# Kernel optimization log

Hardware: AMD Instinct MI355X
Metric: run time of the kernel (lower is better)

Reference implementation:

```python
import jax, jax.numpy as jnp
import numpy as np

H = 12      # num attention heads
W = 128     # one-sided window size (band = 2W+1), also the chunk size
G = 32      # number of global tokens (positions 0..G-1)
NEG = -1e9


def setup_inputs() -> dict:
    key = jax.random.key(0)
    ks = jax.random.split(key, 9)
    B, S, D = 1, 4096, 768
    std = 0.02
    f32 = jnp.float32
    return {
        "hidden_states": jax.random.normal(ks[0], (B, S, D), f32),
        "Wq": jax.random.normal(ks[1], (D, D), f32) * std,
        "bq": jnp.zeros((D,), f32),
        "Wk": jax.random.normal(ks[2], (D, D), f32) * std,
        "bk": jnp.zeros((D,), f32),
        "Wv": jax.random.normal(ks[3], (D, D), f32) * std,
        "bv": jnp.zeros((D,), f32),
        "Wo": jax.random.normal(ks[4], (D, D), f32) * std,
        "bo": jnp.zeros((D,), f32),
    }


def _longformer_attn(hidden, Wq, bq, Wk, bk, Wv, bv, Wo, bo):
    B, S, D = hidden.shape
    dh = D // H
    scale = jnp.asarray(dh, hidden.dtype) ** -0.5

    def proj(Wm, bm):
        return (hidden @ Wm + bm).reshape(B, S, H, dh).transpose(0, 2, 1, 3)  # [B,H,S,dh]

    q = proj(Wq, bq) * scale
    k = proj(Wk, bk)
    v = proj(Wv, bv)

    nc = S // W  # number of query chunks
    q_ch = q.reshape(B, H, nc, W, dh)

    # pad keys/values by one chunk on each side; chunk c sees keys [c*W - W, c*W + 2W)
    kp = jnp.pad(k, ((0, 0), (0, 0), (W, W), (0, 0)))
    vp = jnp.pad(v, ((0, 0), (0, 0), (W, W), (0, 0)))
    idx = (jnp.arange(nc) * W)[:, None] + jnp.arange(3 * W)[None, :]  # [nc, 3W] into padded seq
    k_ch = kp[:, :, idx]  # [B,H,nc,3W,dh]
    v_ch = vp[:, :, idx]

    # banded scores via chunked matmul: [B,H,nc,W,3W]
    band = jnp.einsum('bhcqd,bhckd->bhcqk', q_ch, k_ch)

    # exact band mask |i-j| <= W: with local query qi and local key kj (global j = c*W + kj - W)
    qi = jnp.arange(W)[:, None]           # [W,1]
    kj = jnp.arange(3 * W)[None, :]       # [1,3W]
    in_band = (kj >= qi) & (kj <= qi + 2 * W)                     # [W,3W]
    j = (jnp.arange(nc) * W)[:, None, None] + kj[None] - W        # [nc,1,3W] global key index
    valid = in_band[None] & (j >= G) & (j < S)                    # [nc,W,3W]; j<G handled via global path
    band = jnp.where(valid[None, None], band, NEG)
    band = band.reshape(B, H, S, 3 * W)

    # every query also attends to the G global keys
    gsc = jnp.einsum('bhsd,bhgd->bhsg', q, k[:, :, :G])           # [B,H,S,G]
    scores = jnp.concatenate([gsc, band], axis=-1)                # [B,H,S,G+3W]
    probs = jax.nn.softmax(scores, axis=-1)

    out = jnp.einsum('bhsg,bhgd->bhsd', probs[..., :G], v[:, :, :G])
    pb = probs[..., G:].reshape(B, H, nc, W, 3 * W)
    out = out + jnp.einsum('bhcqk,bhckd->bhcqd', pb, v_ch).reshape(B, H, S, dh)

    # global queries attend to everything (full attention on G rows)
    gq_probs = jax.nn.softmax(jnp.einsum('bhgd,bhsd->bhgs', q[:, :, :G], k), axis=-1)
    out_g = jnp.einsum('bhgs,bhsd->bhgd', gq_probs, v)
    out = out.at[:, :, :G].set(out_g)

    out = out.transpose(0, 2, 1, 3).reshape(B, S, D)
    return out @ Wo + bo


def reference(hidden_states, Wq, bq, Wk, bk, Wv, bv, Wo, bo):
    return _longformer_attn(hidden_states, Wq, bq, Wk, bk, Wv, bv, Wo, bo)
```

## Files before the change

### kernel.cpp

```cpp
#include <hip/hip_runtime.h>
#include <stdint.h>

#define S_LEN 4096
#define DMOD  768
#define NH    12
#define DH    64
#define GG    32
#define NEGBIG (-1e9f)

typedef _Float16 f16;
typedef f16 f16x8 __attribute__((ext_vector_type(8)));
typedef f16 f16x4 __attribute__((ext_vector_type(4)));
typedef float f32x4 __attribute__((ext_vector_type(4)));
typedef uint32_t u32;

#define OFF_H16   ((size_t)0)
#define OFF_WT    ((size_t)6291456)
#define OFF_Q     ((size_t)11010048)
#define OFF_K     ((size_t)17301504)
#define OFF_VT    ((size_t)29884416)
#define OFF_ATT   ((size_t)36175872)
#define OFF_GQO   ((size_t)42467328)
#define OFF_GQL   ((size_t)44040192)

__device__ __forceinline__ void gld_lds16(const void* g, void* l) {
  typedef __attribute__((address_space(3))) u32 lds_u32;
  typedef __attribute__((address_space(1))) u32 glb_u32;
  __builtin_amdgcn_global_load_lds((glb_u32*)(uintptr_t)g,
                                   (lds_u32*)(u32)(uintptr_t)l, 16, 0, 0);
}

__global__ __launch_bounds__(256) void prep_kernel(
    const float* __restrict__ hs,
    const float* __restrict__ Wq, const float* __restrict__ Wk,
    const float* __restrict__ Wv, const float* __restrict__ Wo,
    f16* __restrict__ h16, f16* __restrict__ wt)
{
  const int b = blockIdx.x;
  const int t = threadIdx.x;
  if (b < 576) {
    __shared__ float tile[64][65];
    const int w = b / 144, r2 = b % 144;
    const int n0 = (r2 % 12) * 64, k0 = (r2 / 12) * 64;
    const float* W = (w==0) ? Wq : (w==1) ? Wk : (w==2) ? Wv : Wo;
    f16* WT = wt + (size_t)w * DMOD * DMOD;
    #pragma unroll
    for (int rnd = 0; rnd < 4; ++rnd) {
      const int lin = rnd * 1024 + t * 4;
      const int r = lin >> 6, c = lin & 63;
      const float4 vv = *(const float4*)(W + (size_t)(k0 + r) * DMOD + n0 + c);
      tile[r][c+0] = vv.x; tile[r][c+1] = vv.y; tile[r][c+2] = vv.z; tile[r][c+3] = vv.w;
    }
    __syncthreads();
    #pragma unroll
    for (int rnd = 0; rnd < 2; ++rnd) {
      const int lin = rnd * 256 + t;
      const int n = lin >> 3, kc = (lin & 7) * 8;
      f16x8 o;
      #pragma unroll
      for (int j = 0; j < 8; ++j) o[j] = (f16)tile[kc + j][n];
      *(f16x8*)(WT + (size_t)(n0 + n) * DMOD + k0 + kc) = o;
    }
  } else {
    const size_t idx = (size_t)(b - 576) * 2048 + (size_t)t * 8;
    const float4 a = *(const float4*)(hs + idx);
    const float4 c = *(const float4*)(hs + idx + 4);
    f16x8 o;
    o[0]=(f16)a.x; o[1]=(f16)a.y; o[2]=(f16)a.z; o[3]=(f16)a.w;
    o[4]=(f16)c.x; o[5]=(f16)c.y; o[6]=(f16)c.z; o[7]=(f16)c.w;
    *(f16x8*)(h16 + idx) = o;
  }
}

__global__ __launch_bounds__(256) void gemm_qkv(
    const f16* __restrict__ A, const f16* __restrict__ wt,
    const float* __restrict__ bq, const float* __restrict__ bk, const float* __restrict__ bv,
    f16* __restrict__ q16, f16* __restrict__ k16, f16* __restrict__ vt16)
{
  __shared__ __align__(16) f16 At[3][4096];
  __shared__ __align__(16) f16 Bt[3][4096];
  const int z = blockIdx.z;
  const f16* Wt = wt + (size_t)z * DMOD * DMOD;
  const float* bias = (z==0) ? bq : (z==1) ? bk : bv;
  const float scale = (z==0) ? 0.125f : 1.0f;

  const int tid = threadIdx.x;
  const int lane = tid & 63, wid = tid >> 6;
  const int quad = lane >> 4, l15 = lane & 15;
  const int n0 = blockIdx.x * 128, m0 = blockIdx.y * 128;
  const int wm = (wid >> 1) * 64, wn = (wid & 1) * 64;

  f32x4 acc[4][4];
  #pragma unroll
  for (int i=0;i<4;++i)
    #pragma unroll
    for (int j=0;j<4;++j) acc[i][j] = (f32x4){0.f,0.f,0.f,0.f};

  const int lin0 = tid, lin1 = tid + 256;
  const int ar0 = ((lin0>>6)<<4) + (lin0&15), ac0 = ((lin0>>4)&3)*8;
  const int ar1 = ((lin1>>6)<<4) + (lin1&15), ac1 = ((lin1>>4)&3)*8;
  const f16* Ab = A  + (size_t)m0 * DMOD;
  const f16* Bb = Wt + (size_t)n0 * DMOD;

  #pragma unroll
  for (int p = 0; p < 2; ++p) {
    const int k0 = p * 32;
    gld_lds16(Ab + (size_t)ar0*DMOD + k0 + ac0, &At[p][lin0*8]);
    gld_lds16(Ab + (size_t)ar1*DMOD + k0 + ac1, &At[p][lin1*8]);
    gld_lds16(Bb + (size_t)ar0*DMOD + k0 + ac0, &Bt[p][lin0*8]);
    gld_lds16(Bb + (size_t)ar1*DMOD + k0 + ac1, &Bt[p][lin1*8]);
  }

  #pragma unroll 3
  for (int k = 0; k < 24; ++k) {
    const int cb = k % 3, ib = (k + 2) % 3;
    if (k < 23) {
      asm volatile("s_waitcnt vmcnt(4) lgkmcnt(0)" ::: "memory");
    } else {
      asm volatile("s_waitcnt vmcnt(0) lgkmcnt(0)" ::: "memory");
    }
    __builtin_amdgcn_s_barrier();
    if (k < 22) {
      const int k0 = (k + 2) * 32;
      gld_lds16(Ab + (size_t)ar0*DMOD + k0 + ac0, &At[ib][lin0*8]);
      gld_lds16(Ab + (size_t)ar1*DMOD + k0 + ac1, &At[ib][lin1*8]);
      gld_lds16(Bb + (size_t)ar0*DMOD + k0 + ac0, &Bt[ib][lin0*8]);
      gld_lds16(Bb + (size_t)ar1*DMOD + k0 + ac1, &Bt[ib][lin1*8]);
    }
    f16x8 af[4], bf[4];
    #pragma unroll
    for (int i=0;i<4;++i) {
      af[i] = *(const f16x8*)(&At[cb][((wm>>4)+i)*512 + lane*8]);
      bf[i] = *(const f16x8*)(&Bt[cb][((wn>>4)+i)*512 + lane*8]);
    }
    #pragma unroll
    for (int i=0;i<4;++i)
      #pragma unroll
      for (int j=0;j<4;++j)
        acc[i][j] = __builtin_amdgcn_mfma_f32_16x16x32_f16(af[i], bf[j], acc[i][j], 0, 0, 0);
  }

  if (z < 2) {
    f16* outp = (z==0) ? q16 : k16;
    #pragma unroll
    for (int j=0;j<4;++j) {
      const int col = n0 + wn + j*16 + l15;
      const float bcol = bias[col];
      const int h = col >> 6, d = col & 63;
      #pragma unroll
      for (int i=0;i<4;++i) {
        const int rbase = m0 + wm + i*16 + quad*4;
        f16* dst = outp + ((size_t)h * S_LEN + rbase) * DH + d;
        #pragma unroll
        for (int r=0;r<4;++r)
          dst[(size_t)r * DH] = (f16)((acc[i][j][r] + bcol) * scale);
      }
    }
  } else {
    #pragma unroll
    for (int j=0;j<4;++j) {
      const int col = n0 + wn + j*16 + l15;
      const float bcol = bias[col];
      const int h = col >> 6, d = col & 63;
      #pragma unroll
      for (int i=0;i<4;++i) {
        const int rbase = m0 + wm + i*16 + quad*4;
        f16x4 o;
        #pragma unroll
        for (int r=0;r<4;++r) o[r] = (f16)(acc[i][j][r] + bcol);
        *(f16x4*)(vt16 + ((size_t)h * DH + d) * S_LEN + rbase) = o;
      }
    }
  }
}

__global__ __launch_bounds__(256) void gemm_out(
    const f16* __restrict__ A, const f16* __restrict__ Wt,
    const float* __restrict__ bo, float* __restrict__ outp)
{
  __shared__ __align__(16) f16 At[3][2048];
  __shared__ __align__(16) f16 Bt[3][2048];
  const int tid = threadIdx.x;
  const int lane = tid & 63, wid = tid >> 6;
  const int quad = lane >> 4, l15 = lane & 15;
  const int n0 = blockIdx.x * 64, m0 = blockIdx.y * 64;
  const int wm = (wid >> 1) * 32, wn = (wid & 1) * 32;

  f32x4 acc[2][2];
  #pragma unroll
  for (int i=0;i<2;++i)
    #pragma unroll
    for (int j=0;j<2;++j) acc[i][j] = (f32x4){0.f,0.f,0.f,0.f};

  const int ar = ((tid>>6)<<4) + (tid&15), ac = ((tid>>4)&3)*8;
  const f16* Ab = A  + (size_t)m0 * DMOD;
  const f16* Bb = Wt + (size_t)n0 * DMOD;

  #pragma unroll
  for (int p = 0; p < 2; ++p) {
    const int k0 = p * 32;
    gld_lds16(Ab + (size_t)ar*DMOD + k0 + ac, &At[p][tid*8]);
    gld_lds16(Bb + (size_t)ar*DMOD + k0 + ac, &Bt[p][tid*8]);
  }

  #pragma unroll 3
  for (int k = 0; k < 24; ++k) {
    const int cb = k % 3, ib = (k + 2) % 3;
    if (k < 23) {
      asm volatile("s_waitcnt vmcnt(2) lgkmcnt(0)" ::: "memory");
    } else {
      asm volatile("s_waitcnt vmcnt(0) lgkmcnt(0)" ::: "memory");
    }
    __builtin_amdgcn_s_barrier();
    if (k < 22) {
      const int k0 = (k + 2) * 32;
      gld_lds16(Ab + (size_t)ar*DMOD + k0 + ac, &At[ib][tid*8]);
      gld_lds16(Bb + (size_t)ar*DMOD + k0 + ac, &Bt[ib][tid*8]);
    }
    f16x8 af[2], bf[2];
    #pragma unroll
    for (int i=0;i<2;++i) {
      af[i] = *(const f16x8*)(&At[cb][((wm>>4)+i)*512 + lane*8]);
      bf[i] = *(const f16x8*)(&Bt[cb][((wn>>4)+i)*512 + lane*8]);
    }
    #pragma unroll
    for (int i=0;i<2;++i)
      #pragma unroll
      for (int j=0;j<2;++j)
        acc[i][j] = __builtin_amdgcn_mfma_f32_16x16x32_f16(af[i], bf[j], acc[i][j], 0, 0, 0);
  }

  #pragma unroll
  for (int j=0;j<2;++j) {
    const int col = n0 + wn + j*16 + l15;
    const float bcol = bo[col];
    #pragma unroll
    for (int i=0;i<2;++i) {
      const int rbase = m0 + wm + i*16 + quad*4;
      #pragma unroll
      for (int r=0;r<4;++r)
        outp[(size_t)(rbase + r) * DMOD + col] = acc[i][j][r] + bcol;
    }
  }
}

__global__ __launch_bounds__(256) void band_attn(
    const f16* __restrict__ q16, const f16* __restrict__ k16,
    const f16* __restrict__ vt16, f16* __restrict__ att16,
    float* __restrict__ o_part, float* __restrict__ l_part)
{
  __shared__ __align__(16) f16 Pbuf[4][1280];
  const int h = blockIdx.y;
  const int tid = threadIdx.x, lane = tid & 63, wid = tid >> 6;
  const int quad = lane >> 4, l15 = lane & 15;
  f16* P = &Pbuf[wid][0];

  const int bx = blockIdx.x;
  const bool is_gq = (bx >= 32);
  int gr0 = 0, sp = 0, tcount;
  if (is_gq) {
    sp = (bx - 32) * 4 + wid;
    tcount = 8;
  } else {
    const int sub = bx * 4 + wid;
    if (sub == 0) return;
    gr0 = sub * 32;
    tcount = 10;
  }

  const f16* qh = q16 + (size_t)h * S_LEN * DH;
  const f16* kh = k16 + (size_t)h * S_LEN * DH;
  const f16* vh = vt16 + (size_t)h * DH * S_LEN;

  f16x8 aq[2][2];
  #pragma unroll
  for (int mt=0;mt<2;++mt)
    #pragma unroll
    for (int ks=0;ks<2;++ks)
      aq[mt][ks] = *(const f16x8*)(qh + (size_t)(gr0 + mt*16 + l15)*DH + ks*32 + quad*8);

  f32x4 accO[2][4];
  float lacc[2][4];
  #pragma unroll
  for (int mt=0;mt<2;++mt) {
    #pragma unroll
    for (int n=0;n<4;++n) accO[mt][n] = (f32x4){0.f,0.f,0.f,0.f};
    #pragma unroll
    for (int r=0;r<4;++r) lacc[mt][r] = 0.f;
  }

  for (int t = 0; t < tcount; ++t) {
    int j0;
    if (is_gq) {
      j0 = sp*256 + t*32;
    } else if (t > 0) {
      j0 = gr0 - 128 + (t-1)*32;
      if (j0 <= 0 || j0 >= S_LEN) continue;
    } else {
      j0 = 0;
    }
    f16x8 bk[2][2];
    #pragma unroll
    for (int nt=0;nt<2;++nt) {
      const int key = j0 + nt*16 + l15;
      #pragma unroll
      for (int ks=0;ks<2;++ks)
        bk[nt][ks] = *(const f16x8*)(kh + (size_t)key*DH + ks*32 + quad*8);
    }
    f32x4 sc[2][2];
    #pragma unroll
    for (int mt=0;mt<2;++mt)
      #pragma unroll
      for (int nt=0;nt<2;++nt) {
        f32x4 s = __builtin_amdgcn_mfma_f32_16x16x32_f16(aq[mt][0], bk[nt][0],
                                                         (f32x4){0.f,0.f,0.f,0.f}, 0,0,0);
        sc[mt][nt] = __builtin_amdgcn_mfma_f32_16x16x32_f16(aq[mt][1], bk[nt][1], s, 0,0,0);
      }
    if (!is_gq && (t == 1 || t == 9)) {
      #pragma unroll
      for (int nt=0;nt<2;++nt)
        #pragma unroll
        for (int mt=0;mt<2;++mt)
          #pragma unroll
          for (int r=0;r<4;++r) {
            const int e = (nt*16 + l15) - (mt*16 + quad*4 + r);
            const bool ok = (t == 1) ? (e >= 0) : (e <= 0);
            if (!ok) sc[mt][nt][r] = NEGBIG;
          }
    }
    #pragma unroll
    for (int mt=0;mt<2;++mt)
      #pragma unroll
      for (int r=0;r<4;++r) {
        sc[mt][0][r] = __expf(sc[mt][0][r]);
        sc[mt][1][r] = __expf(sc[mt][1][r]);
        lacc[mt][r] += sc[mt][0][r] + sc[mt][1][r];
      }
    #pragma unroll
    for (int mt=0;mt<2;++mt)
      #pragma unroll
      for (int nt=0;nt<2;++nt)
        #pragma unroll
        for (int r=0;r<4;++r)
          P[(mt*16 + quad*4 + r)*40 + nt*16 + l15] = (f16)sc[mt][nt][r];
    asm volatile("s_waitcnt lgkmcnt(0)" ::: "memory");
    f16x8 ap[2];
    #pragma unroll
    for (int mt=0;mt<2;++mt)
      ap[mt] = *(const f16x8*)(P + (mt*16 + l15)*40 + quad*8);
    #pragma unroll
    for (int n=0;n<4;++n) {
      const f16x8 bv = *(const f16x8*)(vh + (size_t)(n*16 + l15)*S_LEN + j0 + quad*8);
      #pragma unroll
      for (int mt=0;mt<2;++mt)
        accO[mt][n] = __builtin_amdgcn_mfma_f32_16x16x32_f16(ap[mt], bv, accO[mt][n], 0,0,0);
    }
  }

  #pragma unroll
  for (int mt=0;mt<2;++mt)
    #pragma unroll
    for (int r=0;r<4;++r) {
      float v = lacc[mt][r];
      v += __shfl_xor(v, 1, 64);
      v += __shfl_xor(v, 2, 64);
      v += __shfl_xor(v, 4, 64);
      v += __shfl_xor(v, 8, 64);
      lacc[mt][r] = v;
    }

  if (is_gq) {
    const int base = (h*16 + sp)*32;
    #pragma unroll
    for (int mt=0;mt<2;++mt)
      #pragma unroll
      for (int r=0;r<4;++r) {
        const int row = mt*16 + quad*4 + r;
        if (l15 == 0) l_part[base+row] = lacc[mt][r];
        #pragma unroll
        for (int n=0;n<4;++n)
          o_part[(size_t)(base+row)*DH + n*16 + l15] = accO[mt][n][r];
      }
  } else {
    #pragma unroll
    for (int mt=0;mt<2;++mt)
      #pragma unroll
      for (int r=0;r<4;++r) {
        const float inv = 1.f / lacc[mt][r];
        const int s = gr0 + mt*16 + quad*4 + r;
        #pragma unroll
        for (int n=0;n<4;++n)
          att16[(size_t)s * DMOD + h*DH + n*16 + l15] = (f16)(accO[mt][n][r] * inv);
      }
  }
}

__global__ __launch_bounds__(256) void gq_merge(
    const float* __restrict__ o_part, const float* __restrict__ l_part,
    f16* __restrict__ att16)
{
  const int h = blockIdx.x;
  const int t = threadIdx.x;
  for (int u = t; u < 512; u += 256) {
    const int row = u >> 4, c4 = u & 15;
    float4 s = {0.f,0.f,0.f,0.f};
    float l = 0.f;
    for (int sp=0;sp<16;++sp) {
      const int base = (h*16 + sp)*32 + row;
      const float4 v = *(const float4*)&o_part[(size_t)base*DH + c4*4];
      s.x += v.x; s.y += v.y; s.z += v.z; s.w += v.w;
      l += l_part[base];
    }
    const float inv = 1.f / l;
    f16x4 o;
    o[0] = (f16)(s.x*inv); o[1] = (f16)(s.y*inv);
    o[2] = (f16)(s.z*inv); o[3] = (f16)(s.w*inv);
    *(f16x4*)&att16[(size_t)row * DMOD + h*DH + c4*4] = o;
  }
}

extern "C" void kernel_launch(void* const* d_in, const int* in_sizes, int n_in,
                              void* d_out, int out_size, void* d_ws, size_t ws_size,
                              hipStream_t stream)
{
  const float* hs = (const float*)d_in[0];
  const float* Wq = (const float*)d_in[1];
  const float* bq = (const float*)d_in[2];
  const float* Wk = (const float*)d_in[3];
  const float* bk = (const float*)d_in[4];
  const float* Wv = (const float*)d_in[5];
  const float* bv = (const float*)d_in[6];
  const float* Wo = (const float*)d_in[7];
  const float* bo = (const float*)d_in[8];
  float* out = (float*)d_out;
  char* ws = (char*)d_ws;
  f16* h16  = (f16*)(ws + OFF_H16);
  f16* wt   = (f16*)(ws + OFF_WT);
  f16* q16  = (f16*)(ws + OFF_Q);
  f16* k16  = (f16*)(ws + OFF_K);
  f16* vt16 = (f16*)(ws + OFF_VT);
  f16* att16= (f16*)(ws + OFF_ATT);
  float* gqo = (float*)(ws + OFF_GQO);
  float* gql = (float*)(ws + OFF_GQL);

  prep_kernel<<<2112, 256, 0, stream>>>(hs, Wq, Wk, Wv, Wo, h16, wt);
  gemm_qkv<<<dim3(6,32,3), 256, 0, stream>>>(h16, wt, bq, bk, bv, q16, k16, vt16);
  band_attn<<<dim3(36,12), 256, 0, stream>>>(q16, k16, vt16, att16, gqo, gql);
  gq_merge<<<12, 256, 0, stream>>>(gqo, gql, att16);
  gemm_out<<<dim3(12,64), 256, 0, stream>>>(att16, wt + (size_t)3*DMOD*DMOD, bo, out);
}
```

Measured before the change: 170.8 us.

## Widen QKV GEMM tile to 128x256 and remap block indices for L2 locality

The QKV projection GEMM now computes a 128x256 output tile per block instead of 128x128. Each wave accumulates 4x8 MFMA tiles, and the B-operand LDS buffer doubles to hold 256 rows. Block IDs are also remapped so that consecutive blocks group M-rows and share weight columns, which should improve cache reuse. This halves the grid to 288 blocks and roughly doubles the accumulator registers per thread and the LDS footprint, which risks lower occupancy and fewer blocks than CUs to fill the 256 CUs evenly.

After: 175.1 us. 2.5% more time.

```diff
diff --git a/kernel.cpp b/kernel.cpp
--- a/kernel.cpp
+++ b/kernel.cpp
@@ -78,8 +78,13 @@
     f16* __restrict__ q16, f16* __restrict__ k16, f16* __restrict__ vt16)
 {
   __shared__ __align__(16) f16 At[3][4096];
-  __shared__ __align__(16) f16 Bt[3][4096];
-  const int z = blockIdx.z;
+  __shared__ __align__(16) f16 Bt[3][8192];
+
+  const int bid = blockIdx.x + 3*(blockIdx.y + 32*blockIdx.z);
+  const int y  = (bid & 7)*4 + ((bid >> 3) & 3);
+  const int c  = bid >> 5;
+  const int xb = c % 3, z = c / 3;
+
   const f16* Wt = wt + (size_t)z * DMOD * DMOD;
   const float* bias = (z==0) ? bq : (z==1) ? bk : bv;
   const float scale = (z==0) ? 0.125f : 1.0f;
@@ -87,63 +92,73 @@
   const int tid = threadIdx.x;
   const int lane = tid & 63, wid = tid >> 6;
   const int quad = lane >> 4, l15 = lane & 15;
-  const int n0 = blockIdx.x * 128, m0 = blockIdx.y * 128;
-  const int wm = (wid >> 1) * 64, wn = (wid & 1) * 64;
-
-  f32x4 acc[4][4];
+  const int n0 = xb * 256, m0 = y * 128;
+  const int wm = (wid >> 1) * 64, wn = (wid & 1) * 128;
+
+  f32x4 acc[4][8];
   #pragma unroll
   for (int i=0;i<4;++i)
     #pragma unroll
-    for (int j=0;j<4;++j) acc[i][j] = (f32x4){0.f,0.f,0.f,0.f};
-
-  const int lin0 = tid, lin1 = tid + 256;
-  const int ar0 = ((lin0>>6)<<4) + (lin0&15), ac0 = ((lin0>>4)&3)*8;
-  const int ar1 = ((lin1>>6)<<4) + (lin1&15), ac1 = ((lin1>>4)&3)*8;
+    for (int j=0;j<8;++j) acc[i][j] = (f32x4){0.f,0.f,0.f,0.f};
+
+  const int a0 = tid, a1 = tid + 256;
+  const int arA0 = ((a0>>6)<<4) + (a0&15), acA0 = ((a0>>4)&3)*8;
+  const int arA1 = ((a1>>6)<<4) + (a1&15), acA1 = ((a1>>4)&3)*8;
   const f16* Ab = A  + (size_t)m0 * DMOD;
   const f16* Bb = Wt + (size_t)n0 * DMOD;
+  int brow[4], bcolc[4];
+  #pragma unroll
+  for (int q=0;q<4;++q) {
+    const int lin = tid + 256*q;
+    brow[q]  = ((lin>>6)<<4) + (lin&15);
+    bcolc[q] = ((lin>>4)&3)*8;
+  }
 
   #pragma unroll
   for (int p = 0; p < 2; ++p) {
     const int k0 = p * 32;
-    gld_lds16(Ab + (size_t)ar0*DMOD + k0 + ac0, &At[p][lin0*8]);
-    gld_lds16(Ab + (size_t)ar1*DMOD + k0 + ac1, &At[p][lin1*8]);
-    gld_lds16(Bb + (size_t)ar0*DMOD + k0 + ac0, &Bt[p][lin0*8]);
-    gld_lds16(Bb + (size_t)ar1*DMOD + k0 + ac1, &Bt[p][lin1*8]);
+    gld_lds16(Ab + (size_t)arA0*DMOD + k0 + acA0, &At[p][a0*8]);
+    gld_lds16(Ab + (size_t)arA1*DMOD + k0 + acA1, &At[p][a1*8]);
+    #pragma unroll
+    for (int q=0;q<4;++q)
+      gld_lds16(Bb + (size_t)brow[q]*DMOD + k0 + bcolc[q], &Bt[p][(tid+256*q)*8]);
   }
 
   #pragma unroll 3
   for (int k = 0; k < 24; ++k) {
     const int cb = k % 3, ib = (k + 2) % 3;
     if (k < 23) {
-      asm volatile("s_waitcnt vmcnt(4) lgkmcnt(0)" ::: "memory");
+      asm volatile("s_waitcnt vmcnt(6) lgkmcnt(0)" ::: "memory");
     } else {
       asm volatile("s_waitcnt vmcnt(0) lgkmcnt(0)" ::: "memory");
     }
     __builtin_amdgcn_s_barrier();
     if (k < 22) {
       const int k0 = (k + 2) * 32;
-      gld_lds16(Ab + (size_t)ar0*DMOD + k0 + ac0, &At[ib][lin0*8]);
-      gld_lds16(Ab + (size_t)ar1*DMOD + k0 + ac1, &At[ib][lin1*8]);
-      gld_lds16(Bb + (size_t)ar0*DMOD + k0 + ac0, &Bt[ib][lin0*8]);
-      gld_lds16(Bb + (size_t)ar1*DMOD + k0 + ac1, &Bt[ib][lin1*8]);
-    }
-    f16x8 af[4], bf[4];
-    #pragma unroll
-    for (int i=0;i<4;++i) {
+      gld_lds16(Ab + (size_t)arA0*DMOD + k0 + acA0, &At[ib][a0*8]);
+      gld_lds16(Ab + (size_t)arA1*DMOD + k0 + acA1, &At[ib][a1*8]);
+      #pragma unroll
+      for (int q=0;q<4;++q)
+        gld_lds16(Bb + (size_t)brow[q]*DMOD + k0 + bcolc[q], &Bt[ib][(tid+256*q)*8]);
+    }
+    f16x8 af[4], bf[8];
+    #pragma unroll
+    for (int i=0;i<4;++i)
       af[i] = *(const f16x8*)(&At[cb][((wm>>4)+i)*512 + lane*8]);
-      bf[i] = *(const f16x8*)(&Bt[cb][((wn>>4)+i)*512 + lane*8]);
-    }
+    #pragma unroll
+    for (int j=0;j<8;++j)
+      bf[j] = *(const f16x8*)(&Bt[cb][((wn>>4)+j)*512 + lane*8]);
     #pragma unroll
     for (int i=0;i<4;++i)
       #pragma unroll
-      for (int j=0;j<4;++j)
+      for (int j=0;j<8;++j)
         acc[i][j] = __builtin_amdgcn_mfma_f32_16x16x32_f16(af[i], bf[j], acc[i][j], 0, 0, 0);
   }
 
   if (z < 2) {
     f16* outp = (z==0) ? q16 : k16;
     #pragma unroll
-    for (int j=0;j<4;++j) {
+    for (int j=0;j<8;++j) {
       const int col = n0 + wn + j*16 + l15;
       const float bcol = bias[col];
       const int h = col >> 6, d = col & 63;
@@ -158,7 +173,7 @@
     }
   } else {
     #pragma unroll
-    for (int j=0;j<4;++j) {
+    for (int j=0;j<8;++j) {
       const int col = n0 + wn + j*16 + l15;
       const float bcol = bias[col];
       const int h = col >> 6, d = col & 63;
@@ -444,7 +459,7 @@
   float* gql = (float*)(ws + OFF_GQL);
 
   prep_kernel<<<2112, 256, 0, stream>>>(hs, Wq, Wk, Wv, Wo, h16, wt);
-  gemm_qkv<<<dim3(6,32,3), 256, 0, stream>>>(h16, wt, bq, bk, bv, q16, k16, vt16);
+  gemm_qkv<<<dim3(3,32,3), 256, 0, stream>>>(h16, wt, bq, bk, bv, q16, k16, vt16);
   band_attn<<<dim3(36,12), 256, 0, stream>>>(q16, k16, vt16, att16, gqo, gql);
   gq_merge<<<12, 256, 0, stream>>>(gqo, gql, att16);
   gemm_out<<<dim3(12,64), 256, 0, stream>>>(att16, wt + (size_t)3*DMOD*DMOD, bo, out);
```

## Replace LDS-staged GEMM pipelines with direct global-to-register MFMA fragment loads

Applied to the files above, without the earlier changes.

Both projection GEMMs drop the shared-memory triple buffer with global_load_lds and barriers. Each wave now loads its MFMA fragments straight from global memory into registers, double-buffered with vmcnt waits. The output GEMM is retiled to 32x128 blocks of 128 threads, and the QKV grid is flattened to 2D. This removes LDS traffic and block-wide synchronisation, but data is no longer shared across waves through LDS, so redundant global/L2 reads rise.

Result: slower. 211.7 us (+23.9%).

```diff
diff --git a/kernel.cpp b/kernel.cpp
--- a/kernel.cpp
+++ b/kernel.cpp
@@ -23,13 +23,6 @@
 #define OFF_GQO   ((size_t)42467328)
 #define OFF_GQL   ((size_t)44040192)
 
-__device__ __forceinline__ void gld_lds16(const void* g, void* l) {
-  typedef __attribute__((address_space(3))) u32 lds_u32;
-  typedef __attribute__((address_space(1))) u32 glb_u32;
-  __builtin_amdgcn_global_load_lds((glb_u32*)(uintptr_t)g,
-                                   (lds_u32*)(u32)(uintptr_t)l, 16, 0, 0);
-}
-
 __global__ __launch_bounds__(256) void prep_kernel(
     const float* __restrict__ hs,
     const float* __restrict__ Wq, const float* __restrict__ Wk,
@@ -77,18 +70,26 @@
     const float* __restrict__ bq, const float* __restrict__ bk, const float* __restrict__ bv,
     f16* __restrict__ q16, f16* __restrict__ k16, f16* __restrict__ vt16)
 {
-  __shared__ __align__(16) f16 At[3][4096];
-  __shared__ __align__(16) f16 Bt[3][4096];
-  const int z = blockIdx.z;
-  const f16* Wt = wt + (size_t)z * DMOD * DMOD;
-  const float* bias = (z==0) ? bq : (z==1) ? bk : bv;
-  const float scale = (z==0) ? 0.125f : 1.0f;
-
   const int tid = threadIdx.x;
   const int lane = tid & 63, wid = tid >> 6;
   const int quad = lane >> 4, l15 = lane & 15;
-  const int n0 = blockIdx.x * 128, m0 = blockIdx.y * 128;
+  const int xb = blockIdx.x;
+  const int m0 = blockIdx.y * 128;
   const int wm = (wid >> 1) * 64, wn = (wid & 1) * 64;
+  const int z  = xb / 6;
+  const int n0 = (xb % 6) * 128;
+
+  const float* bias = (z==0) ? bq : (z==1) ? bk : bv;
+  const float scale = (z==0) ? 0.125f : 1.0f;
+
+  const f16* pa[4];
+  const f16* pb[4];
+  #pragma unroll
+  for (int i=0;i<4;++i)
+    pa[i] = A + (size_t)(m0 + wm + i*16 + l15) * DMOD + quad*8;
+  #pragma unroll
+  for (int j=0;j<4;++j)
+    pb[j] = wt + (size_t)(xb*128 + wn + j*16 + l15) * DMOD + quad*8;
 
   f32x4 acc[4][4];
   #pragma unroll
@@ -96,48 +97,36 @@
     #pragma unroll
     for (int j=0;j<4;++j) acc[i][j] = (f32x4){0.f,0.f,0.f,0.f};
 
-  const int lin0 = tid, lin1 = tid + 256;
-  const int ar0 = ((lin0>>6)<<4) + (lin0&15), ac0 = ((lin0>>4)&3)*8;
-  const int ar1 = ((lin1>>6)<<4) + (lin1&15), ac1 = ((lin1>>4)&3)*8;
-  const f16* Ab = A  + (size_t)m0 * DMOD;
-  const f16* Bb = Wt + (size_t)n0 * DMOD;
-
-  #pragma unroll
-  for (int p = 0; p < 2; ++p) {
-    const int k0 = p * 32;
-    gld_lds16(Ab + (size_t)ar0*DMOD + k0 + ac0, &At[p][lin0*8]);
-    gld_lds16(Ab + (size_t)ar1*DMOD + k0 + ac1, &At[p][lin1*8]);
-    gld_lds16(Bb + (size_t)ar0*DMOD + k0 + ac0, &Bt[p][lin0*8]);
-    gld_lds16(Bb + (size_t)ar1*DMOD + k0 + ac1, &Bt[p][lin1*8]);
-  }
-
-  #pragma unroll 3
-  for (int k = 0; k < 24; ++k) {
-    const int cb = k % 3, ib = (k + 2) % 3;
-    if (k < 23) {
-      asm volatile("s_waitcnt vmcnt(4) lgkmcnt(0)" ::: "memory");
+  f16x8 cu[8], nx[8];
+  #pragma unroll
+  for (int i=0;i<4;++i) { cu[i] = *(const f16x8*)(pa[i]); cu[4+i] = *(const f16x8*)(pb[i]); }
+
+  #pragma unroll
+  for (int k = 0; k < 24; k += 2) {
+    {
+      const int ko = (k+1)*32;
+      #pragma unroll
+      for (int i=0;i<4;++i) { nx[i] = *(const f16x8*)(pa[i] + ko); nx[4+i] = *(const f16x8*)(pb[i] + ko); }
+    }
+    asm volatile("s_waitcnt vmcnt(8)" ::: "memory");
+    #pragma unroll
+    for (int i=0;i<4;++i)
+      #pragma unroll
+      for (int j=0;j<4;++j)
+        acc[i][j] = __builtin_amdgcn_mfma_f32_16x16x32_f16(cu[i], cu[4+j], acc[i][j], 0,0,0);
+    if (k + 2 < 24) {
+      const int ko = (k+2)*32;
+      #pragma unroll
+      for (int i=0;i<4;++i) { cu[i] = *(const f16x8*)(pa[i] + ko); cu[4+i] = *(const f16x8*)(pb[i] + ko); }
+      asm volatile("s_waitcnt vmcnt(8)" ::: "memory");
     } else {
-      asm volatile("s_waitcnt vmcnt(0) lgkmcnt(0)" ::: "memory");
-    }
-    __builtin_amdgcn_s_barrier();
-    if (k < 22) {
-      const int k0 = (k + 2) * 32;
-      gld_lds16(Ab + (size_t)ar0*DMOD + k0 + ac0, &At[ib][lin0*8]);
-      gld_lds16(Ab + (size_t)ar1*DMOD + k0 + ac1, &At[ib][lin1*8]);
-      gld_lds16(Bb + (size_t)ar0*DMOD + k0 + ac0, &Bt[ib][lin0*8]);
-      gld_lds16(Bb + (size_t)ar1*DMOD + k0 + ac1, &Bt[ib][lin1*8]);
-    }
-    f16x8 af[4], bf[4];
-    #pragma unroll
-    for (int i=0;i<4;++i) {
-      af[i] = *(const f16x8*)(&At[cb][((wm>>4)+i)*512 + lane*8]);
-      bf[i] = *(const f16x8*)(&Bt[cb][((wn>>4)+i)*512 + lane*8]);
+      asm volatile("s_waitcnt vmcnt(0)" ::: "memory");
     }
     #pragma unroll
     for (int i=0;i<4;++i)
       #pragma unroll
       for (int j=0;j<4;++j)
-        acc[i][j] = __builtin_amdgcn_mfma_f32_16x16x32_f16(af[i], bf[j], acc[i][j], 0, 0, 0);
+        acc[i][j] = __builtin_amdgcn_mfma_f32_16x16x32_f16(nx[i], nx[4+j], acc[i][j], 0,0,0);
   }
 
   if (z < 2) {
@@ -174,69 +163,76 @@
   }
 }
 
-__global__ __launch_bounds__(256) void gemm_out(
+__global__ __launch_bounds__(128) void gemm_out(
     const f16* __restrict__ A, const f16* __restrict__ Wt,
     const float* __restrict__ bo, float* __restrict__ outp)
 {
-  __shared__ __align__(16) f16 At[3][2048];
-  __shared__ __align__(16) f16 Bt[3][2048];
   const int tid = threadIdx.x;
   const int lane = tid & 63, wid = tid >> 6;
   const int quad = lane >> 4, l15 = lane & 15;
-  const int n0 = blockIdx.x * 64, m0 = blockIdx.y * 64;
-  const int wm = (wid >> 1) * 32, wn = (wid & 1) * 32;
-
-  f32x4 acc[2][2];
+  const int n0 = blockIdx.x * 128, m0 = blockIdx.y * 32;
+  const int wn = wid * 64;
+
+  const f16* pa[2];
+  const f16* pb[4];
   #pragma unroll
   for (int i=0;i<2;++i)
-    #pragma unroll
-    for (int j=0;j<2;++j) acc[i][j] = (f32x4){0.f,0.f,0.f,0.f};
-
-  const int ar = ((tid>>6)<<4) + (tid&15), ac = ((tid>>4)&3)*8;
-  const f16* Ab = A  + (size_t)m0 * DMOD;
-  const f16* Bb = Wt + (size_t)n0 * DMOD;
-
-  #pragma unroll
-  for (int p = 0; p < 2; ++p) {
-    const int k0 = p * 32;
-    gld_lds16(Ab + (size_t)ar*DMOD + k0 + ac, &At[p][tid*8]);
-    gld_lds16(Bb + (size_t)ar*DMOD + k0 + ac, &Bt[p][tid*8]);
-  }
-
-  #pragma unroll 3
-  for (int k = 0; k < 24; ++k) {
-    const int cb = k % 3, ib = (k + 2) % 3;
-    if (k < 23) {
-      asm volatile("s_waitcnt vmcnt(2) lgkmcnt(0)" ::: "memory");
+    pa[i] = A + (size_t)(m0 + i*16 + l15) * DMOD + quad*8;
+  #pragma unroll
+  for (int j=0;j<4;++j)
+    pb[j] = Wt + (size_t)(n0 + wn + j*16 + l15) * DMOD + quad*8;
+
+  f32x4 acc[2][4];
+  #pragma unroll
+  for (int i=0;i<2;++i)
+    #pragma unroll
+    for (int j=0;j<4;++j) acc[i][j] = (f32x4){0.f,0.f,0.f,0.f};
+
+  f16x8 cu[6], nx[6];
+  #pragma unroll
+  for (int i=0;i<2;++i) cu[i] = *(const f16x8*)(pa[i]);
+  #pragma unroll
+  for (int j=0;j<4;++j) cu[2+j] = *(const f16x8*)(pb[j]);
+
+  #pragma unroll
+  for (int k = 0; k < 24; k += 2) {
+    {
+      const int ko = (k+1)*32;
+      #pragma unroll
+      for (int i=0;i<2;++i) nx[i] = *(const f16x8*)(pa[i] + ko);
+      #pragma unroll
+      for (int j=0;j<4;++j) nx[2+j] = *(const f16x8*)(pb[j] + ko);
+    }
+    asm volatile("s_waitcnt vmcnt(6)" ::: "memory");
+    #pragma unroll
+    for (int i=0;i<2;++i)
+      #pragma unroll
+      for (int j=0;j<4;++j)
+        acc[i][j] = __builtin_amdgcn_mfma_f32_16x16x32_f16(cu[i], cu[2+j], acc[i][j], 0,0,0);
+    if (k + 2 < 24) {
+      const int ko = (k+2)*32;
+      #pragma unroll
+      for (int i=0;i<2;++i) cu[i] = *(const f16x8*)(pa[i] + ko);
+      #pragma unroll
+      for (int j=0;j<4;++j) cu[2+j] = *(const f16x8*)(pb[j] + ko);
+      asm volatile("s_waitcnt vmcnt(6)" ::: "memory");
     } else {
-      asm volatile("s_waitcnt vmcnt(0) lgkmcnt(0)" ::: "memory");
-    }
-    __builtin_amdgcn_s_barrier();
-    if (k < 22) {
-      const int k0 = (k + 2) * 32;
-      gld_lds16(Ab + (size_t)ar*DMOD + k0 + ac, &At[ib][tid*8]);
-      gld_lds16(Bb + (size_t)ar*DMOD + k0 + ac, &Bt[ib][tid*8]);
-    }
-    f16x8 af[2], bf[2];
-    #pragma unroll
-    for (int i=0;i<2;++i) {
-      af[i] = *(const f16x8*)(&At[cb][((wm>>4)+i)*512 + lane*8]);
-      bf[i] = *(const f16x8*)(&Bt[cb][((wn>>4)+i)*512 + lane*8]);
+      asm volatile("s_waitcnt vmcnt(0)" ::: "memory");
     }
     #pragma unroll
     for (int i=0;i<2;++i)
       #pragma unroll
-      for (int j=0;j<2;++j)
-        acc[i][j] = __builtin_amdgcn_mfma_f32_16x16x32_f16(af[i], bf[j], acc[i][j], 0, 0, 0);
-  }
-
-  #pragma unroll
-  for (int j=0;j<2;++j) {
+      for (int j=0;j<4;++j)
+        acc[i][j] = __builtin_amdgcn_mfma_f32_16x16x32_f16(nx[i], nx[2+j], acc[i][j], 0,0,0);
+  }
+
+  #pragma unroll
+  for (int j=0;j<4;++j) {
     const int col = n0 + wn + j*16 + l15;
     const float bcol = bo[col];
     #pragma unroll
     for (int i=0;i<2;++i) {
-      const int rbase = m0 + wm + i*16 + quad*4;
+      const int rbase = m0 + i*16 + quad*4;
       #pragma unroll
       for (int r=0;r<4;++r)
         outp[(size_t)(rbase + r) * DMOD + col] = acc[i][j][r] + bcol;
@@ -444,8 +440,8 @@
   float* gql = (float*)(ws + OFF_GQL);
 
   prep_kernel<<<2112, 256, 0, stream>>>(hs, Wq, Wk, Wv, Wo, h16, wt);
-  gemm_qkv<<<dim3(6,32,3), 256, 0, stream>>>(h16, wt, bq, bk, bv, q16, k16, vt16);
+  gemm_qkv<<<dim3(18,32), 256, 0, stream>>>(h16, wt, bq, bk, bv, q16, k16, vt16);
   band_attn<<<dim3(36,12), 256, 0, stream>>>(q16, k16, vt16, att16, gqo, gql);
   gq_merge<<<12, 256, 0, stream>>>(gqo, gql, att16);
-  gemm_out<<<dim3(12,64), 256, 0, stream>>>(att16, wt + (size_t)3*DMOD*DMOD, bo, out);
-}
+  gemm_out<<<dim3(6,128), 128, 0, stream>>>(att16, wt + (size_t)3*DMOD*DMOD, bo, out);
+}
```
